# Kernel optimization log

Measured on AMD Instinct MI355X. Metric: run time of the kernel, lower is better.

The kernel has to match this reference:

```python
import jax, jax.numpy as jnp
import numpy as np

B = 1024
D = 64          # embed_dim (symp == dise)
H1, H2 = 8, 8   # dsd metapath fanouts
U1, U2, U3 = 8, 8, 16  # usu metapath fanouts
NUM_SYMP = 50000
NUM_DISE = 2000
NEG_SLOPE = 0.2


def setup_inputs() -> dict:
    key = jax.random.key(0)
    ks = jax.random.split(key, 16)
    s = 0.05
    E_s = jax.random.normal(ks[0], (NUM_SYMP + 1, D), jnp.float32) * s
    E_d = jax.random.normal(ks[1], (NUM_DISE + 1, D), jnp.float32) * s
    # padding_idx=0 rows are zero in torch Embedding
    E_s = E_s.at[0].set(0.0)
    E_d = E_d.at[0].set(0.0)
    W = lambda k: jax.random.normal(k, (D, D), jnp.float32) * (1.0 / np.sqrt(D))
    return {
        "E_s": E_s,
        "E_d": E_d,
        "W_dsd_21": W(ks[2]),
        "W_dsd_22": W(ks[3]),
        "W_dsd_11": W(ks[4]),
        "W_dsd_12": W(ks[5]),
        "W_usu_3": W(ks[6]),
        "W_usu_21": W(ks[7]),
        "W_usu_22": W(ks[8]),
        "W_usu_1": W(ks[9]),
        "label": jax.random.randint(ks[10], (B,), 0, NUM_DISE + 1),
        "dsd_1": jax.random.randint(ks[11], (B, H1), 0, NUM_SYMP + 1),
        "dsd_2": jax.random.randint(ks[12], (B, H1, H2), 0, NUM_DISE + 1),
        "usu_1": jax.random.randint(ks[13], (B, U1), 0, NUM_SYMP + 1),
        "usu_2": jax.random.randint(ks[14], (B, U1, U2), 0, 10000),
        "usu_3": jax.random.randint(ks[15], (B, U1, U2, U3), 0, NUM_SYMP + 1),
    }


def _avg_real(msg, idx):
    # mean over the neighbor axis, counting only nonzero (real) neighbors;
    # zero output if all neighbors are padding (matches weight==1e8 -> 0)
    cnt = (idx != 0).sum(-1).astype(msg.dtype)
    w = jnp.where(cnt > 0, 1.0 / (cnt + 1e-8), 0.0)
    return msg.sum(-2) * w[..., None]


def _leaky(x):
    return jax.nn.leaky_relu(x, NEG_SLOPE)


def reference(E_s, E_d, W_dsd_21, W_dsd_22, W_dsd_11, W_dsd_12,
              W_usu_3, W_usu_21, W_usu_22, W_usu_1,
              label, dsd_1, dsd_2, usu_1, usu_2, usu_3):
    # ---- forward_dsd (eval mode: dropout = identity) ----
    td = E_d[label]                       # [B, D]
    es = E_s[dsd_1]                       # [B, H1, D]
    ed = E_d[dsd_2]                       # [B, H1, H2, D]
    m_sd = ed @ W_dsd_21.T + (ed * es[:, :, None, :]) @ W_dsd_22.T
    m_sd = _avg_real(m_sd, dsd_2)         # [B, H1, D]
    m_ss = es @ W_dsd_21.T                # [B, H1, D]
    emb_s1 = _leaky(m_ss + m_sd)          # [B, H1, D]
    m_ds = emb_s1 @ W_dsd_11.T + (emb_s1 * td[:, None, :]) @ W_dsd_12.T
    m_ds = _avg_real(m_ds, dsd_1)         # [B, D]
    emb_dise = _leaky(m_ds + td @ W_dsd_11.T)

    # ---- forward_usu ----
    u1 = E_s[usu_1]                       # [B, U1, D]
    s3 = E_s[usu_3]                       # [B, U1, U2, U3, D]
    m_us3 = _avg_real(s3 @ W_usu_3.T, usu_3)   # [B, U1, U2, D]
    eu2 = _leaky(m_us3)                   # [B, U1, U2, D]
    m_su = eu2 @ W_usu_21.T + (eu2 * u1[:, :, None, :]) @ W_usu_22.T
    m_su = _avg_real(m_su, usu_2)         # [B, U1, D]
    m_ss_u = u1 @ W_usu_21.T              # [B, U1, D]
    es1 = _leaky(m_ss_u + m_su)           # [B, U1, D]
    emb_user = _leaky(_avg_real(es1 @ W_usu_1.T, usu_1))  # [B, D]

    pred_score = (emb_dise * emb_user).sum(-1)  # [B]
    return pred_score
```

## Files before the change

kernel.cpp:

```cpp
#include <hip/hip_runtime.h>
#include <hip/hip_bf16.h>


typedef __attribute__((ext_vector_type(8))) short short8;
typedef __attribute__((ext_vector_type(8))) unsigned short ushort8;
typedef __attribute__((ext_vector_type(4))) float f32x4;

__device__ __forceinline__ int rfl(int v) { return __builtin_amdgcn_readfirstlane(v); }
__device__ __forceinline__ float bcastf(float v, int l) {
    return __int_as_float(__builtin_amdgcn_readlane(__float_as_int(v), l));
}
__device__ __forceinline__ float leakyf(float x) { return x >= 0.f ? x : 0.2f * x; }

__device__ __forceinline__ unsigned short bf16bits(float x) {
    __hip_bfloat16 h = __float2bfloat16(x);
    return __builtin_bit_cast(unsigned short, h);
}
__device__ __forceinline__ float bf16tof(unsigned short s) {
    __hip_bfloat16 h = __builtin_bit_cast(__hip_bfloat16, s);
    return __bfloat162float(h);
}
__device__ __forceinline__ float bflo(unsigned int u) {
    return __uint_as_float(u << 16);
}
__device__ __forceinline__ float bfhi(unsigned int u) {
    return __uint_as_float(u & 0xffff0000u);
}

__device__ __forceinline__ void stage_w512(float* dst, const float* __restrict__ W, int tid) {
#pragma unroll
    for (int c = 0; c < 2; ++c) {
        int f4 = c * 512 + tid;
        int j = f4 >> 4, g = f4 & 15;
        float4 v = reinterpret_cast<const float4*>(W)[f4];
        reinterpret_cast<float4*>(dst)[(j << 4) + ((g + j) & 15)] = v;
    }
}

__device__ __forceinline__ float dot1_lds(float x, const float* w, int lane) {
    float a0 = 0.f, a1 = 0.f, a2 = 0.f, a3 = 0.f;
#pragma unroll
    for (int g = 0; g < 16; ++g) {
        float4 c = reinterpret_cast<const float4*>(w)[(lane << 4) + ((g + lane) & 15)];
        int k = 4 * g;
        a0 = fmaf(bcastf(x, k + 0), c.x, a0);
        a1 = fmaf(bcastf(x, k + 1), c.y, a1);
        a2 = fmaf(bcastf(x, k + 2), c.z, a2);
        a3 = fmaf(bcastf(x, k + 3), c.w, a3);
    }
    return (a0 + a1) + (a2 + a3);
}

__device__ __forceinline__ float dot2_lds(float xs, float xm,
                                          const float* w1, const float* w2, int lane) {
    float a0 = 0.f, a1 = 0.f, a2 = 0.f, a3 = 0.f;
#pragma unroll
    for (int g = 0; g < 16; ++g) {
        int f4 = (lane << 4) + ((g + lane) & 15);
        float4 c1 = reinterpret_cast<const float4*>(w1)[f4];
        float4 c2 = reinterpret_cast<const float4*>(w2)[f4];
        int k = 4 * g;
        float s0 = bcastf(xs, k + 0), s1 = bcastf(xs, k + 1);
        float s2 = bcastf(xs, k + 2), s3 = bcastf(xs, k + 3);
        float m0 = bcastf(xm, k + 0), m1 = bcastf(xm, k + 1);
        float m2 = bcastf(xm, k + 2), m3 = bcastf(xm, k + 3);
        a0 = fmaf(s0, c1.x, a0); a1 = fmaf(m0, c2.x, a1);
        a2 = fmaf(s1, c1.y, a2); a3 = fmaf(m1, c2.y, a3);
        a0 = fmaf(s2, c1.z, a0); a1 = fmaf(m2, c2.z, a1);
        a2 = fmaf(s3, c1.w, a2); a3 = fmaf(m3, c2.w, a3);
    }
    return (a0 + a1) + (a2 + a3);
}

__global__ __launch_bounds__(256) void k_cvt(const float* __restrict__ E_s,
                                             unsigned short* __restrict__ T) {
    int t = blockIdx.x * 256 + threadIdx.x;
    if (t >= 400008) return;
    const float4* p = reinterpret_cast<const float4*>(E_s) + (size_t)t * 2;
    float4 a = p[0], b = p[1];
    ushort8 o;
    o[0] = bf16bits(a.x); o[1] = bf16bits(a.y); o[2] = bf16bits(a.z); o[3] = bf16bits(a.w);
    o[4] = bf16bits(b.x); o[5] = bf16bits(b.y); o[6] = bf16bits(b.z); o[7] = bf16bits(b.w);
    *(reinterpret_cast<ushort8*>(T) + t) = o;
}

#define XP 72

__global__ __launch_bounds__(512, 6) void k_main(
    const float* __restrict__ E_s, const unsigned short* __restrict__ Ebf,
    const float* __restrict__ E_d,
    const float* __restrict__ W21, const float* __restrict__ W22,
    const float* __restrict__ W11, const float* __restrict__ W12,
    const float* __restrict__ W3, const float* __restrict__ W21u,
    const float* __restrict__ W22u, const float* __restrict__ W1u,
    const int* __restrict__ label, const int* __restrict__ dsd_1,
    const int* __restrict__ dsd_2, const int* __restrict__ usu_1,
    const int* __restrict__ usu_2, const int* __restrict__ usu_3,
    float* __restrict__ emb_dise, float* __restrict__ emb_user)
{
    __shared__ float4 smraw[3328];
    const int tid = threadIdx.x, lane = tid & 63, w = rfl(tid >> 6);

    if (blockIdx.x < 1024) {
        const int b = blockIdx.x;
        unsigned short* sXb  = (unsigned short*)smraw;
        unsigned short* sW3b = sXb + 64 * XP;
        float* sW21 = (float*)(sW3b + 64 * XP);
        float* sW22 = sW21 + 4096;
        float* sA2  = sW22 + 4096;

        const int sub = lane >> 4;
        const int cg  = lane & 15;

        int idv[8];
#pragma unroll
        for (int i = 0; i < 8; ++i)
            idv[i] = usu_3[((size_t)(b * 64 + w * 8 + i)) * 16 + cg];

        {
            int row = tid >> 3, c0 = (tid & 7) << 3;
            const float* src = W3 + row * 64 + c0;
#pragma unroll
            for (int i = 0; i < 8; ++i)
                sW3b[row * XP + c0 + i] = bf16bits(src[i]);
        }
        stage_w512(sW21, W21u, tid);
        stage_w512(sW22, W22u, tid);

#pragma unroll 2
        for (int i = 0; i < 8; ++i) {
            int ql = w * 8 + i;
            unsigned long long nzm = __ballot(idv[i] != 0) & 0xFFFFull;
            int cnt = (int)__popcll(nzm);
            float wgt = cnt > 0 ? 1.f / ((float)cnt + 1e-8f) : 0.f;
            float a0 = 0.f, a1 = 0.f, a2 = 0.f, a3 = 0.f;
#pragma unroll
            for (int k = 0; k < 4; ++k) {
                int id = __shfl(idv[i], k * 4 + sub, 64);
                uint2 v = *reinterpret_cast<const uint2*>(Ebf + (size_t)id * 64 + cg * 4);
                a0 += bflo(v.x); a1 += bfhi(v.x);
                a2 += bflo(v.y); a3 += bfhi(v.y);
            }
            a0 += __shfl_xor(a0, 16, 64); a1 += __shfl_xor(a1, 16, 64);
            a2 += __shfl_xor(a2, 16, 64); a3 += __shfl_xor(a3, 16, 64);
            a0 += __shfl_xor(a0, 32, 64); a1 += __shfl_xor(a1, 32, 64);
            a2 += __shfl_xor(a2, 32, 64); a3 += __shfl_xor(a3, 32, 64);
            a0 *= wgt; a1 *= wgt; a2 *= wgt; a3 *= wgt;
            unsigned int p0 = ((unsigned int)bf16bits(a1) << 16) | bf16bits(a0);
            unsigned int p1 = ((unsigned int)bf16bits(a3) << 16) | bf16bits(a2);
            if (sub == 0) {
                uint2 st; st.x = p0; st.y = p1;
                *reinterpret_cast<uint2*>(sXb + ql * XP + cg * 4) = st;
            }
        }
        __syncthreads();

        {
            const int m = lane & 15, quad = lane >> 4;
            const int wt = w >> 1, J0 = (w & 1) * 2;
            const int base = (16 * wt + m) * XP + quad * 8;
            short8 a0 = *(const short8*)(sXb + base);
            short8 a1 = *(const short8*)(sXb + base + 32);
            int cp0 = 0, cp1 = 0;
            const int* m2 = usu_2 + (b * 8 + 2 * wt) * 8;
#pragma unroll
            for (int u = 0; u < 8; ++u) { cp0 += (m2[u] != 0); cp1 += (m2[u + 8] != 0); }
            float wg0 = cp0 > 0 ? 1.f / ((float)cp0 + 1e-8f) : 0.f;
            float wg1 = cp1 > 0 ? 1.f / ((float)cp1 + 1e-8f) : 0.f;
#pragma unroll
            for (int jj = 0; jj < 2; ++jj) {
                int J = J0 + jj;
                const int wb = (16 * J + m) * XP + quad * 8;
                short8 b0 = *(const short8*)(sW3b + wb);
                short8 b1 = *(const short8*)(sW3b + wb + 32);
                f32x4 acc = {0.f, 0.f, 0.f, 0.f};
                acc = __builtin_amdgcn_mfma_f32_16x16x32_bf16(a0, b0, acc, 0, 0, 0);
                acc = __builtin_amdgcn_mfma_f32_16x16x32_bf16(a1, b1, acc, 0, 0, 0);
                float t = leakyf(acc[0]) + leakyf(acc[1]) + leakyf(acc[2]) + leakyf(acc[3]);
                t += __shfl_xor(t, 16, 64);
                if (quad == 0) sA2[(2 * wt + 0) * 64 + J * 16 + m] = t * wg0;
                if (quad == 2) sA2[(2 * wt + 1) * 64 + J * 16 + m] = t * wg1;
            }
        }
        __syncthreads();

        stage_w512((float*)sXb, W1u, tid);
        {
            int p = w;
            float x = sA2[p * 64 + lane];
            float u1e = E_s[(size_t)usu_1[b * 8 + p] * 64 + lane];
            float y = leakyf(dot2_lds(x + u1e, x * u1e, sW21, sW22, lane));
            sA2[p * 64 + lane] = y;
        }
        __syncthreads();

        if (w == 0) {
            float sE = 0.f; int cnt = 0;
            const int* u1i = usu_1 + b * 8;
#pragma unroll
            for (int h = 0; h < 8; ++h) {
                sE += sA2[h * 64 + lane];
                cnt += (u1i[h] != 0);
            }
            float wgt = cnt > 0 ? 1.f / ((float)cnt + 1e-8f) : 0.f;
            float eu = leakyf(dot1_lds(sE * wgt, (float*)sXb, lane));
            emb_user[(size_t)b * 64 + lane] = eu;
        }
    } else {
        const int b0 = (blockIdx.x - 1024) * 4;
        float* sW1 = (float*)smraw;
        float* sW2 = sW1 + 4096;
        float* sS1 = sW2 + 4096;

        stage_w512(sW1, W21, tid);
        stage_w512(sW2, W22, tid);
        __syncthreads();

#pragma unroll
        for (int i = 0; i < 4; ++i) {
            int rl = w * 4 + i;
            int row = b0 * 8 + rl;
            int is = dsd_1[row];
            float es = E_s[(size_t)is * 64 + lane];
            const int* d2 = dsd_2 + row * 8;
            float sA = 0.f; int cnt = 0;
#pragma unroll
            for (int h = 0; h < 8; ++h) {
                int id = d2[h];
                cnt += (id != 0);
                sA += E_d[(size_t)id * 64 + lane];
            }
            float wgt = cnt > 0 ? 1.f / ((float)cnt + 1e-8f) : 0.f;
            float A = sA * wgt;
            sS1[rl * 64 + lane] = leakyf(dot2_lds(A + es, A * es, sW1, sW2, lane));
        }
        __syncthreads();
        stage_w512(sW1, W11, tid);
        stage_w512(sW2, W12, tid);
        __syncthreads();

        if (w < 4) {
            int b = b0 + w;
            float sE = 0.f; int cnt = 0;
            const int* d1 = dsd_1 + b * 8;
#pragma unroll
            for (int h = 0; h < 8; ++h) {
                sE += sS1[(w * 8 + h) * 64 + lane];
                cnt += (d1[h] != 0);
            }
            float wgt = cnt > 0 ? 1.f / ((float)cnt + 1e-8f) : 0.f;
            float A3 = sE * wgt;
            float td = E_d[(size_t)label[b] * 64 + lane];
            emb_dise[(size_t)b * 64 + lane] = leakyf(dot2_lds(A3 + td, A3 * td, sW1, sW2, lane));
        }
    }
}

__global__ __launch_bounds__(256) void k_dot(const float* __restrict__ ed,
                                             const float* __restrict__ eu,
                                             float* __restrict__ out) {
    const int lane = threadIdx.x & 63;
    const int b = rfl((int)((blockIdx.x * blockDim.x + threadIdx.x) >> 6));
    float pr = ed[(size_t)b * 64 + lane] * eu[(size_t)b * 64 + lane];
#pragma unroll
    for (int off = 32; off > 0; off >>= 1) pr += __shfl_down(pr, off, 64);
    if (lane == 0) out[b] = pr;
}

extern "C" void kernel_launch(void* const* d_in, const int* in_sizes, int n_in,
                              void* d_out, int out_size, void* d_ws, size_t ws_size,
                              hipStream_t stream) {
    const float* E_s  = (const float*)d_in[0];
    const float* E_d  = (const float*)d_in[1];
    const float* W_dsd_21 = (const float*)d_in[2];
    const float* W_dsd_22 = (const float*)d_in[3];
    const float* W_dsd_11 = (const float*)d_in[4];
    const float* W_dsd_12 = (const float*)d_in[5];
    const float* W_usu_3  = (const float*)d_in[6];
    const float* W_usu_21 = (const float*)d_in[7];
    const float* W_usu_22 = (const float*)d_in[8];
    const float* W_usu_1  = (const float*)d_in[9];
    const int* label = (const int*)d_in[10];
    const int* dsd_1 = (const int*)d_in[11];
    const int* dsd_2 = (const int*)d_in[12];
    const int* usu_1 = (const int*)d_in[13];
    const int* usu_2 = (const int*)d_in[14];
    const int* usu_3 = (const int*)d_in[15];
    float* out = (float*)d_out;

    unsigned short* Ebf = (unsigned short*)d_ws;
    float* emb_dise = (float*)((char*)d_ws + 6400128);
    float* emb_user = emb_dise + 1024 * 64;

    k_cvt<<<1563, 256, 0, stream>>>(E_s, Ebf);
    k_main<<<1280, 512, 0, stream>>>(E_s, Ebf, E_d,
                                     W_dsd_21, W_dsd_22, W_dsd_11, W_dsd_12,
                                     W_usu_3, W_usu_21, W_usu_22, W_usu_1,
                                     label, dsd_1, dsd_2, usu_1, usu_2, usu_3,
                                     emb_dise, emb_user);
    k_dot<<<256, 256, 0, stream>>>(emb_dise, emb_user, out);
}
```

Measured before the change: 122.9 us.

## Replace fp32 LDS matvecs with bf16 MFMA tiles for paired weight products

The per-row fp32 dot products against W21/W22 and W11/W12, which used readlane broadcasts, become bf16 MFMA 16x16x32 tiles. Both the usu and dsd branches first stage the sum and product operands and the weights as padded bf16 in LDS. This is meant to cut VALU and LDS work in the small matmul stages. It also shrinks the shared-memory footprint, which could allow more resident blocks. The cost is bf16 rounding in these stages and extra barriers and staging passes.

```diff
diff --git a/kernel.cpp b/kernel.cpp
--- a/kernel.cpp
+++ b/kernel.cpp
@@ -16,16 +16,8 @@
     __hip_bfloat16 h = __float2bfloat16(x);
     return __builtin_bit_cast(unsigned short, h);
 }
-__device__ __forceinline__ float bf16tof(unsigned short s) {
-    __hip_bfloat16 h = __builtin_bit_cast(__hip_bfloat16, s);
-    return __bfloat162float(h);
-}
-__device__ __forceinline__ float bflo(unsigned int u) {
-    return __uint_as_float(u << 16);
-}
-__device__ __forceinline__ float bfhi(unsigned int u) {
-    return __uint_as_float(u & 0xffff0000u);
-}
+__device__ __forceinline__ float bflo(unsigned int u) { return __uint_as_float(u << 16); }
+__device__ __forceinline__ float bfhi(unsigned int u) { return __uint_as_float(u & 0xffff0000u); }
 
 __device__ __forceinline__ void stage_w512(float* dst, const float* __restrict__ W, int tid) {
 #pragma unroll
@@ -47,27 +39,6 @@
         a1 = fmaf(bcastf(x, k + 1), c.y, a1);
         a2 = fmaf(bcastf(x, k + 2), c.z, a2);
         a3 = fmaf(bcastf(x, k + 3), c.w, a3);
-    }
-    return (a0 + a1) + (a2 + a3);
-}
-
-__device__ __forceinline__ float dot2_lds(float xs, float xm,
-                                          const float* w1, const float* w2, int lane) {
-    float a0 = 0.f, a1 = 0.f, a2 = 0.f, a3 = 0.f;
-#pragma unroll
-    for (int g = 0; g < 16; ++g) {
-        int f4 = (lane << 4) + ((g + lane) & 15);
-        float4 c1 = reinterpret_cast<const float4*>(w1)[f4];
-        float4 c2 = reinterpret_cast<const float4*>(w2)[f4];
-        int k = 4 * g;
-        float s0 = bcastf(xs, k + 0), s1 = bcastf(xs, k + 1);
-        float s2 = bcastf(xs, k + 2), s3 = bcastf(xs, k + 3);
-        float m0 = bcastf(xm, k + 0), m1 = bcastf(xm, k + 1);
-        float m2 = bcastf(xm, k + 2), m3 = bcastf(xm, k + 3);
-        a0 = fmaf(s0, c1.x, a0); a1 = fmaf(m0, c2.x, a1);
-        a2 = fmaf(s1, c1.y, a2); a3 = fmaf(m1, c2.y, a3);
-        a0 = fmaf(s2, c1.z, a0); a1 = fmaf(m2, c2.z, a1);
-        a2 = fmaf(s3, c1.w, a2); a3 = fmaf(m3, c2.w, a3);
     }
     return (a0 + a1) + (a2 + a3);
 }
@@ -85,6 +56,29 @@
 }
 
 #define XP 72
+
+__device__ __forceinline__ f32x4 pair_mfma(
+    const unsigned short* sXs, const unsigned short* sXm,
+    const unsigned short* sWb1, const unsigned short* sWb2,
+    int arow, int brow, int quad)
+{
+    const int ab = arow * XP + quad * 8;
+    const int bb = brow * XP + quad * 8;
+    short8 as0 = *(const short8*)(sXs + ab);
+    short8 as1 = *(const short8*)(sXs + ab + 32);
+    short8 am0 = *(const short8*)(sXm + ab);
+    short8 am1 = *(const short8*)(sXm + ab + 32);
+    short8 b10 = *(const short8*)(sWb1 + bb);
+    short8 b11 = *(const short8*)(sWb1 + bb + 32);
+    short8 b20 = *(const short8*)(sWb2 + bb);
+    short8 b21 = *(const short8*)(sWb2 + bb + 32);
+    f32x4 acc = {0.f, 0.f, 0.f, 0.f};
+    acc = __builtin_amdgcn_mfma_f32_16x16x32_bf16(as0, b10, acc, 0, 0, 0);
+    acc = __builtin_amdgcn_mfma_f32_16x16x32_bf16(as1, b11, acc, 0, 0, 0);
+    acc = __builtin_amdgcn_mfma_f32_16x16x32_bf16(am0, b20, acc, 0, 0, 0);
+    acc = __builtin_amdgcn_mfma_f32_16x16x32_bf16(am1, b21, acc, 0, 0, 0);
+    return acc;
+}
 
 __global__ __launch_bounds__(512, 6) void k_main(
     const float* __restrict__ E_s, const unsigned short* __restrict__ Ebf,
@@ -98,19 +92,22 @@
     const int* __restrict__ usu_2, const int* __restrict__ usu_3,
     float* __restrict__ emb_dise, float* __restrict__ emb_user)
 {
-    __shared__ float4 smraw[3328];
+    __shared__ float4 smraw[2560];
     const int tid = threadIdx.x, lane = tid & 63, w = rfl(tid >> 6);
+    const int m_ = lane & 15, quad = lane >> 4;
 
     if (blockIdx.x < 1024) {
         const int b = blockIdx.x;
-        unsigned short* sXb  = (unsigned short*)smraw;
-        unsigned short* sW3b = sXb + 64 * XP;
-        float* sW21 = (float*)(sW3b + 64 * XP);
-        float* sW22 = sW21 + 4096;
-        float* sA2  = sW22 + 4096;
-
-        const int sub = lane >> 4;
-        const int cg  = lane & 15;
+        unsigned short* sXb   = (unsigned short*)smraw;
+        unsigned short* sW3b  = sXb + 4608;
+        unsigned short* sW21b = sW3b + 4608;
+        unsigned short* sW22b = sW21b + 4608;
+        float* sA2  = (float*)(sW22b + 4608);
+        float* sES1 = sA2 + 512;
+        unsigned short* sXs = sXb;
+        unsigned short* sXm = sXb + 16 * XP;
+
+        const int sub = lane >> 4, cg = lane & 15;
 
         int idv[8];
 #pragma unroll
@@ -119,13 +116,16 @@
 
         {
             int row = tid >> 3, c0 = (tid & 7) << 3;
-            const float* src = W3 + row * 64 + c0;
-#pragma unroll
-            for (int i = 0; i < 8; ++i)
-                sW3b[row * XP + c0 + i] = bf16bits(src[i]);
-        }
-        stage_w512(sW21, W21u, tid);
-        stage_w512(sW22, W22u, tid);
+            const float* p3 = W3 + row * 64 + c0;
+            const float* p1 = W21u + row * 64 + c0;
+            const float* p2 = W22u + row * 64 + c0;
+#pragma unroll
+            for (int i = 0; i < 8; ++i) {
+                sW3b[row * XP + c0 + i]  = bf16bits(p3[i]);
+                sW21b[row * XP + c0 + i] = bf16bits(p1[i]);
+                sW22b[row * XP + c0 + i] = bf16bits(p2[i]);
+            }
+        }
 
 #pragma unroll 2
         for (int i = 0; i < 8; ++i) {
@@ -156,9 +156,8 @@
         __syncthreads();
 
         {
-            const int m = lane & 15, quad = lane >> 4;
             const int wt = w >> 1, J0 = (w & 1) * 2;
-            const int base = (16 * wt + m) * XP + quad * 8;
+            const int base = (16 * wt + m_) * XP + quad * 8;
             short8 a0 = *(const short8*)(sXb + base);
             short8 a1 = *(const short8*)(sXb + base + 32);
             int cp0 = 0, cp1 = 0;
@@ -170,7 +169,7 @@
 #pragma unroll
             for (int jj = 0; jj < 2; ++jj) {
                 int J = J0 + jj;
-                const int wb = (16 * J + m) * XP + quad * 8;
+                const int wb = (16 * J + m_) * XP + quad * 8;
                 short8 b0 = *(const short8*)(sW3b + wb);
                 short8 b1 = *(const short8*)(sW3b + wb + 32);
                 f32x4 acc = {0.f, 0.f, 0.f, 0.f};
@@ -178,20 +177,32 @@
                 acc = __builtin_amdgcn_mfma_f32_16x16x32_bf16(a1, b1, acc, 0, 0, 0);
                 float t = leakyf(acc[0]) + leakyf(acc[1]) + leakyf(acc[2]) + leakyf(acc[3]);
                 t += __shfl_xor(t, 16, 64);
-                if (quad == 0) sA2[(2 * wt + 0) * 64 + J * 16 + m] = t * wg0;
-                if (quad == 2) sA2[(2 * wt + 1) * 64 + J * 16 + m] = t * wg1;
-            }
-        }
-        __syncthreads();
-
-        stage_w512((float*)sXb, W1u, tid);
+                if (quad == 0) sA2[(2 * wt + 0) * 64 + J * 16 + m_] = t * wg0;
+                if (quad == 2) sA2[(2 * wt + 1) * 64 + J * 16 + m_] = t * wg1;
+            }
+        }
+        __syncthreads();
+
         {
             int p = w;
             float x = sA2[p * 64 + lane];
             float u1e = E_s[(size_t)usu_1[b * 8 + p] * 64 + lane];
-            float y = leakyf(dot2_lds(x + u1e, x * u1e, sW21, sW22, lane));
-            sA2[p * 64 + lane] = y;
-        }
+            sXs[p * XP + lane] = bf16bits(x + u1e);
+            sXm[p * XP + lane] = bf16bits(x * u1e);
+        }
+        __syncthreads();
+
+        if (w < 4) {
+            f32x4 acc = pair_mfma(sXs, sXm, sW21b, sW22b, m_, 16 * w + m_, quad);
+            if (quad < 2) {
+#pragma unroll
+                for (int r = 0; r < 4; ++r)
+                    sES1[(quad * 4 + r) * 64 + w * 16 + m_] = leakyf(acc[r]);
+            }
+        }
+        __syncthreads();
+
+        stage_w512((float*)sW21b, W1u, tid);
         __syncthreads();
 
         if (w == 0) {
@@ -199,22 +210,31 @@
             const int* u1i = usu_1 + b * 8;
 #pragma unroll
             for (int h = 0; h < 8; ++h) {
-                sE += sA2[h * 64 + lane];
+                sE += sES1[h * 64 + lane];
                 cnt += (u1i[h] != 0);
             }
             float wgt = cnt > 0 ? 1.f / ((float)cnt + 1e-8f) : 0.f;
-            float eu = leakyf(dot1_lds(sE * wgt, (float*)sXb, lane));
+            float eu = leakyf(dot1_lds(sE * wgt, (float*)sW21b, lane));
             emb_user[(size_t)b * 64 + lane] = eu;
         }
     } else {
         const int b0 = (blockIdx.x - 1024) * 4;
-        float* sW1 = (float*)smraw;
-        float* sW2 = sW1 + 4096;
-        float* sS1 = sW2 + 4096;
-
-        stage_w512(sW1, W21, tid);
-        stage_w512(sW2, W22, tid);
-        __syncthreads();
+        unsigned short* sXs   = (unsigned short*)smraw;
+        unsigned short* sXm   = sXs + 2304;
+        unsigned short* sW21b = sXm + 2304;
+        unsigned short* sW22b = sW21b + 4608;
+        float* sS1 = (float*)(sW22b + 4608);
+
+        {
+            int row = tid >> 3, c0 = (tid & 7) << 3;
+            const float* p1 = W21 + row * 64 + c0;
+            const float* p2 = W22 + row * 64 + c0;
+#pragma unroll
+            for (int i = 0; i < 8; ++i) {
+                sW21b[row * XP + c0 + i] = bf16bits(p1[i]);
+                sW22b[row * XP + c0 + i] = bf16bits(p2[i]);
+            }
+        }
 
 #pragma unroll
         for (int i = 0; i < 4; ++i) {
@@ -232,17 +252,25 @@
             }
             float wgt = cnt > 0 ? 1.f / ((float)cnt + 1e-8f) : 0.f;
             float A = sA * wgt;
-            sS1[rl * 64 + lane] = leakyf(dot2_lds(A + es, A * es, sW1, sW2, lane));
-        }
-        __syncthreads();
-        stage_w512(sW1, W11, tid);
-        stage_w512(sW2, W12, tid);
+            sXs[rl * XP + lane] = bf16bits(A + es);
+            sXm[rl * XP + lane] = bf16bits(A * es);
+        }
+        __syncthreads();
+
+        {
+            const int Mt = w >> 2, J = w & 3;
+            f32x4 acc = pair_mfma(sXs, sXm, sW21b, sW22b,
+                                  16 * Mt + m_, 16 * J + m_, quad);
+#pragma unroll
+            for (int r = 0; r < 4; ++r)
+                sS1[(16 * Mt + quad * 4 + r) * 64 + J * 16 + m_] = leakyf(acc[r]);
+        }
         __syncthreads();
 
         if (w < 4) {
-            int b = b0 + w;
+            int bb = b0 + w;
             float sE = 0.f; int cnt = 0;
-            const int* d1 = dsd_1 + b * 8;
+            const int* d1 = dsd_1 + bb * 8;
 #pragma unroll
             for (int h = 0; h < 8; ++h) {
                 sE += sS1[(w * 8 + h) * 64 + lane];
@@ -250,8 +278,29 @@
             }
             float wgt = cnt > 0 ? 1.f / ((float)cnt + 1e-8f) : 0.f;
             float A3 = sE * wgt;
-            float td = E_d[(size_t)label[b] * 64 + lane];
-            emb_dise[(size_t)b * 64 + lane] = leakyf(dot2_lds(A3 + td, A3 * td, sW1, sW2, lane));
+            float td = E_d[(size_t)label[bb] * 64 + lane];
+            sXs[w * XP + lane] = bf16bits(A3 + td);
+            sXm[w * XP + lane] = bf16bits(A3 * td);
+        } else {
+            int t2 = tid - 256;
+            int row = t2 >> 2, c0 = (t2 & 3) << 4;
+            const float* p1 = W11 + row * 64 + c0;
+            const float* p2 = W12 + row * 64 + c0;
+#pragma unroll
+            for (int i = 0; i < 16; ++i) {
+                sW21b[row * XP + c0 + i] = bf16bits(p1[i]);
+                sW22b[row * XP + c0 + i] = bf16bits(p2[i]);
+            }
+        }
+        __syncthreads();
+
+        if (w < 4) {
+            f32x4 acc = pair_mfma(sXs, sXm, sW21b, sW22b, m_, 16 * w + m_, quad);
+            if (quad == 0) {
+#pragma unroll
+                for (int r = 0; r < 4; ++r)
+                    emb_dise[(size_t)(b0 + r) * 64 + w * 16 + m_] = leakyf(acc[r]);
+            }
         }
     }
 }
```

After: 115.6 us, median of 2. 6.0% less time.
